# Optimization experiments

Hardware: AMD Instinct MI355X
Metric: run time of the kernel (lower is better)

## Reference

```python
import jax, jax.numpy as jnp
import numpy as np

B, N, F = 8, 1024, 512
H, D = 4, 128  # num_heads, output_dim
LEAKY_ALPHA = 0.2
MASK_VAL = -1e10


def setup_inputs() -> dict:
    key = jax.random.key(0)
    ks = jax.random.split(key, 6)
    X = jax.random.normal(ks[0], (B, N, F), dtype=jnp.float32)
    A = (jax.random.uniform(ks[1], (B, N, N)) < 0.05).astype(jnp.float32)
    A = jnp.maximum(A, jnp.eye(N, dtype=jnp.float32)[None])
    W_att = jax.random.normal(ks[2], (H, F, D), dtype=jnp.float32) * (1.0 / np.sqrt(F))
    a_att = jax.random.normal(ks[3], (H, 2, D), dtype=jnp.float32) * (1.0 / np.sqrt(D))
    kernel = jax.random.normal(ks[4], (H, F, D), dtype=jnp.float32) * (1.0 / np.sqrt(F))
    bias = jax.random.normal(ks[5], (H * D,), dtype=jnp.float32) * 0.02
    return {"X": X, "A": A, "W_att": W_att, "a_att": a_att, "kernel": kernel, "bias": bias}


def reference(X, A, W_att, a_att, kernel, bias):
    # Per-head feature projection used only for attention scores: [H,B,N,D]
    xf = jnp.einsum('bnf,hfd->hbnd', X, W_att)
    att_self = jnp.einsum('hbnd,hd->hbn', xf, a_att[:, 0])       # [H,B,N]
    att_neigh = jnp.einsum('hbnd,hd->hbn', xf, a_att[:, 1])      # [H,B,N]
    # additive scores: scores[h,b,i,j] = self[i] + neigh[j]
    scores = att_self[..., :, None] + att_neigh[..., None, :]    # [H,B,N,N]
    scores = jnp.where(scores >= 0, scores, LEAKY_ALPHA * scores)
    scores = scores + MASK_VAL * (1.0 - A)[None]                 # adjacency mask
    attn = jax.nn.softmax(scores, axis=-1)                       # [H,B,N,N]
    # aggregate raw features X, then per-head kernel projection
    agg = jnp.einsum('hbij,bjf->hbif', attn, X)                  # [H,B,N,F]
    out = jnp.einsum('hbnf,hfd->bnhd', agg, kernel)              # [B,N,H,D]
    out = out.reshape(out.shape[0], out.shape[1], -1)            # concat heads -> [B,N,H*D]
    out = out + bias
    return jax.nn.elu(out)
```

## Files before the change

kernel.cpp:

```cpp
#include <hip/hip_runtime.h>
#include <hip/hip_bf16.h>
#include <math.h>

namespace {
constexpr int B = 8, N = 1024, F = 512, H = 4, D = 128, HD = H * D;
constexpr int ROWS = B * N;
constexpr float LEAKY = 0.2f;

constexpr size_t UV_OFF  = 0;
constexpr size_t ATT_OFF = 4096;
constexpr size_t Y_OFF   = 69632;
constexpr size_t XB_OFF  = 2166784;
constexpr size_t WKB_OFF = 4263936;
}

typedef __attribute__((ext_vector_type(8))) short short8;
typedef __attribute__((ext_vector_type(4))) float f32x4;

__device__ __forceinline__ ushort bf16bits(float x) {
    __hip_bfloat16 h = __float2bfloat16(x);
    return *reinterpret_cast<ushort*>(&h);
}
__device__ __forceinline__ float blo(uint u) {
    return __uint_as_float(u << 16);
}
__device__ __forceinline__ float bhi(uint u) {
    return __uint_as_float(u & 0xffff0000u);
}

extern "C" __global__ __launch_bounds__(256) void k_pre(
    const float* __restrict__ Watt, const float* __restrict__ aatt,
    const float* __restrict__ Wk, float* __restrict__ uv,
    __hip_bfloat16* __restrict__ Wkb) {
    __shared__ ushort T[128][136];
    if (blockIdx.x < 16) {
        int h = blockIdx.x >> 2, f0 = (blockIdx.x & 3) * 128;
#pragma unroll
        for (int p = 0; p < 16; ++p) {
            int fi = p * 8 + (threadIdx.x >> 5);
            int d4 = (threadIdx.x & 31) * 4;
            float4 v = *reinterpret_cast<const float4*>(
                Wk + ((size_t)h * F + f0 + fi) * D + d4);
            T[d4 + 0][fi] = bf16bits(v.x);
            T[d4 + 1][fi] = bf16bits(v.y);
            T[d4 + 2][fi] = bf16bits(v.z);
            T[d4 + 3][fi] = bf16bits(v.w);
        }
        __syncthreads();
        int d = threadIdx.x >> 1, hf = threadIdx.x & 1;
        ushort* dst =
            (ushort*)Wkb + (size_t)(h * 128 + d) * F + f0 + hf * 64;
        const ushort* src = &T[d][hf * 64];
#pragma unroll
        for (int q = 0; q < 8; ++q)
            *reinterpret_cast<uint4*>(dst + q * 8) =
                *reinterpret_cast<const uint4*>(src + q * 8);
    } else {
        int t = (blockIdx.x - 16) * 256 + threadIdx.x;
        int f = t % F;
        int h = (t / F) % H;
        int w = t / (F * H);
        const float* Wrow = Watt + (size_t)(h * F + f) * D;
        const float* arow = aatt + (size_t)(h * 2 + w) * D;
        float s = 0.f;
#pragma unroll 4
        for (int d = 0; d < D; ++d) s = fmaf(Wrow[d], arow[d], s);
        uv[(size_t)w * (H * F) + h * F + f] = s;
    }
}

extern "C" __global__ __launch_bounds__(256) void k_att(
    const float* __restrict__ X, const float* __restrict__ uv,
    float* __restrict__ att, __hip_bfloat16* __restrict__ Xb) {
    int wave = threadIdx.x >> 6, lane = threadIdx.x & 63;
    int row = blockIdx.x * 4 + wave;
    const float4* xr = reinterpret_cast<const float4*>(X + (size_t)row * F);
    float4 v0 = xr[lane * 2], v1 = xr[lane * 2 + 1];

    union { short8 s; __hip_bfloat16 h[8]; } pk;
    pk.h[0] = __float2bfloat16(v0.x); pk.h[1] = __float2bfloat16(v0.y);
    pk.h[2] = __float2bfloat16(v0.z); pk.h[3] = __float2bfloat16(v0.w);
    pk.h[4] = __float2bfloat16(v1.x); pk.h[5] = __float2bfloat16(v1.y);
    pk.h[6] = __float2bfloat16(v1.z); pk.h[7] = __float2bfloat16(v1.w);
    *reinterpret_cast<short8*>(Xb + (size_t)row * F + lane * 8) = pk.s;

    float acc[2][H];
#pragma unroll
    for (int w = 0; w < 2; ++w)
#pragma unroll
        for (int h = 0; h < H; ++h) {
            const float4* up = reinterpret_cast<const float4*>(
                uv + (size_t)w * (H * F) + h * F + lane * 8);
            float4 u0 = up[0], u1 = up[1];
            float a = 0.f;
            a = fmaf(v0.x, u0.x, a); a = fmaf(v0.y, u0.y, a);
            a = fmaf(v0.z, u0.z, a); a = fmaf(v0.w, u0.w, a);
            a = fmaf(v1.x, u1.x, a); a = fmaf(v1.y, u1.y, a);
            a = fmaf(v1.z, u1.z, a); a = fmaf(v1.w, u1.w, a);
            acc[w][h] = a;
        }
#pragma unroll
    for (int w = 0; w < 2; ++w)
#pragma unroll
        for (int h = 0; h < H; ++h) {
            float v = acc[w][h];
#pragma unroll
            for (int off = 32; off > 0; off >>= 1) v += __shfl_xor(v, off);
            if (lane == 0) att[(size_t)w * (H * ROWS) + h * ROWS + row] = v;
        }
}

extern "C" __global__ __launch_bounds__(256) void k_gemm(
    const __hip_bfloat16* __restrict__ Xb,
    const __hip_bfloat16* __restrict__ Wkb,
    __hip_bfloat16* __restrict__ Y) {
    __shared__ __align__(16) char smem[16384];
    int tid = threadIdx.x;
    int lane = tid & 63, wv = tid >> 6;
    int wr = wv >> 1, wc = wv & 1;
    int lt = (blockIdx.x & 7) * 128 + (blockIdx.x >> 3);
    int bm = lt >> 3, bn = lt & 7;
    int row0 = bm * 64, col0 = bn * 64;

    const ushort* Ag = (const ushort*)Xb;
    const ushort* Bg = (const ushort*)Wkb;

    int aoff[2][2], boff[2][2];
#pragma unroll
    for (int ks = 0; ks < 2; ++ks) {
        int cb = ks * 4 + (lane >> 4);
#pragma unroll
        for (int i = 0; i < 2; ++i) {
            int ra = wr * 32 + i * 16 + (lane & 15);
            aoff[i][ks] = ra * 128 + (cb ^ (ra & 7)) * 16;
            int rb = wc * 32 + i * 16 + (lane & 15);
            boff[i][ks] = 8192 + rb * 128 + (cb ^ (rb & 7)) * 16;
        }
    }
    int srow[2], sgb[2];
#pragma unroll
    for (int i = 0; i < 2; ++i) {
        srow[i] = i * 32 + wv * 8 + (lane >> 3);
        sgb[i] = (lane & 7) ^ (srow[i] & 7);
    }

    f32x4 acc[2][2] = {};
    for (int k0 = 0; k0 < F; k0 += 64) {
        __syncthreads();
#pragma unroll
        for (int i = 0; i < 2; ++i) {
            const ushort* ga = Ag + (size_t)(row0 + srow[i]) * F + k0 + sgb[i] * 8;
            __builtin_amdgcn_global_load_lds(
                (const __attribute__((address_space(1))) uint32_t*)ga,
                (__attribute__((address_space(3))) uint32_t*)(smem + wv * 1024 + i * 4096),
                16, 0, 0);
            const ushort* gb = Bg + (size_t)(col0 + srow[i]) * F + k0 + sgb[i] * 8;
            __builtin_amdgcn_global_load_lds(
                (const __attribute__((address_space(1))) uint32_t*)gb,
                (__attribute__((address_space(3))) uint32_t*)(smem + 8192 + wv * 1024 + i * 4096),
                16, 0, 0);
        }
        __syncthreads();
#pragma unroll
        for (int ks = 0; ks < 2; ++ks) {
            short8 af[2], bf[2];
#pragma unroll
            for (int i = 0; i < 2; ++i) {
                af[i] = *reinterpret_cast<short8*>(smem + aoff[i][ks]);
                bf[i] = *reinterpret_cast<short8*>(smem + boff[i][ks]);
            }
#pragma unroll
            for (int mi = 0; mi < 2; ++mi)
#pragma unroll
                for (int ni = 0; ni < 2; ++ni)
                    acc[mi][ni] = __builtin_amdgcn_mfma_f32_16x16x32_bf16(
                        af[mi], bf[ni], acc[mi][ni], 0, 0, 0);
        }
    }
    int cr = (lane >> 4) * 4, cc = lane & 15;
#pragma unroll
    for (int mi = 0; mi < 2; ++mi)
#pragma unroll
        for (int ni = 0; ni < 2; ++ni) {
            int gr = row0 + wr * 32 + mi * 16 + cr;
            int gc = col0 + wc * 32 + ni * 16 + cc;
#pragma unroll
            for (int r = 0; r < 4; ++r)
                Y[(size_t)(gr + r) * HD + gc] =
                    __float2bfloat16(acc[mi][ni][r]);
        }
}

extern "C" __global__ __launch_bounds__(256) void k_attn_agg(
    const float* __restrict__ A, const float* __restrict__ att,
    const ushort* __restrict__ Y, const float* __restrict__ bias,
    float* __restrict__ out) {
    int g = blockIdx.x;
    int bi = ((g & 7) << 10) | (g >> 3);
    int b = bi >> 10;
    int tid = threadIdx.x;
    int lane = tid & 63, wv = tid >> 6;
    __shared__ int idxs[N];
    __shared__ int2 ent[H][256];
    __shared__ int wsum[4];

    const float* Arow = A + (size_t)bi * N;
    float4 av = *reinterpret_cast<const float4*>(Arow + tid * 4);
    int cnt = (av.x != 0.f) + (av.y != 0.f) + (av.z != 0.f) + (av.w != 0.f);
    int isc = cnt;
#pragma unroll
    for (int off = 1; off < 64; off <<= 1) {
        int t = __shfl_up(isc, off);
        if (lane >= off) isc += t;
    }
    if (lane == 63) wsum[wv] = isc;
    __syncthreads();
    int prefix = 0;
#pragma unroll
    for (int wj = 0; wj < 4; ++wj) prefix += (wj < wv) ? wsum[wj] : 0;
    int nnz = wsum[0] + wsum[1] + wsum[2] + wsum[3];
    int wo = prefix + isc - cnt;
    int jb = tid * 4;
    if (av.x != 0.f) idxs[wo++] = jb;
    if (av.y != 0.f) idxs[wo++] = jb + 1;
    if (av.z != 0.f) idxs[wo++] = jb + 2;
    if (av.w != 0.f) idxs[wo++] = jb + 3;
    __syncthreads();

    int h = wv;
    int grp = lane >> 4, sub = lane & 15;
    float sself = att[(size_t)h * ROWS + bi];
    const float* nrow = att + (size_t)(H + h) * ROWS + (size_t)b * N;
    const char* Ybyte = (const char*)(Y + ((size_t)b * N) * HD + h * D + sub * 8);

    float m = -1e30f, l = 0.f;
    float acc[8] = {};
    for (int c0 = 0; c0 < nnz; c0 += 256) {
        int cn = min(256, nnz - c0);
        int kpad = (cn + 15) & ~15;
        float lm = -1e30f;
        for (int k = lane; k < cn; k += 64) {
            int idx = idxs[c0 + k];
            float s = sself + nrow[idx];
            s = s >= 0.f ? s : LEAKY * s;
            ent[h][k] = make_int2(idx << 10, __float_as_int(s));
            lm = fmaxf(lm, s);
        }
        for (int k = cn + lane; k < kpad; k += 64) ent[h][k] = make_int2(0, 0);
#pragma unroll
        for (int off = 32; off > 0; off >>= 1)
            lm = fmaxf(lm, __shfl_xor(lm, off));
        float mn = fmaxf(m, lm);
        float scale = __expf(m - mn);
        float ls = 0.f;
        for (int k = lane; k < cn; k += 64) {
            int2 p = ent[h][k];
            float e = __expf(__int_as_float(p.y) - mn);
            ent[h][k].y = __float_as_int(e);
            ls += e;
        }
#pragma unroll
        for (int off = 32; off > 0; off >>= 1) ls += __shfl_xor(ls, off);
        l = fmaf(l, scale, ls);
#pragma unroll
        for (int q = 0; q < 8; ++q) acc[q] *= scale;
        m = mn;
        for (int k = 0; k < kpad; k += 16) {
            int2 p[4];
#pragma unroll
            for (int q = 0; q < 4; ++q) p[q] = ent[h][k + q * 4 + grp];
            uint4 y[4];
#pragma unroll
            for (int q = 0; q < 4; ++q)
                y[q] = *reinterpret_cast<const uint4*>(Ybyte + (size_t)(uint)p[q].x);
#pragma unroll
            for (int q = 0; q < 4; ++q) {
                float w = __int_as_float(p[q].y);
                acc[0] = fmaf(w, blo(y[q].x), acc[0]);
                acc[1] = fmaf(w, bhi(y[q].x), acc[1]);
                acc[2] = fmaf(w, blo(y[q].y), acc[2]);
                acc[3] = fmaf(w, bhi(y[q].y), acc[3]);
                acc[4] = fmaf(w, blo(y[q].z), acc[4]);
                acc[5] = fmaf(w, bhi(y[q].z), acc[5]);
                acc[6] = fmaf(w, blo(y[q].w), acc[6]);
                acc[7] = fmaf(w, bhi(y[q].w), acc[7]);
            }
        }
    }
#pragma unroll
    for (int q = 0; q < 8; ++q) {
        acc[q] += __shfl_xor(acc[q], 16);
        acc[q] += __shfl_xor(acc[q], 32);
    }
    if (grp == 0) {
        float inv = 1.f / l;
        int cbase = h * D + sub * 8;
        float4 b0 = *reinterpret_cast<const float4*>(bias + cbase);
        float4 b1 = *reinterpret_cast<const float4*>(bias + cbase + 4);
        float o[8];
        o[0] = acc[0] * inv + b0.x; o[1] = acc[1] * inv + b0.y;
        o[2] = acc[2] * inv + b0.z; o[3] = acc[3] * inv + b0.w;
        o[4] = acc[4] * inv + b1.x; o[5] = acc[5] * inv + b1.y;
        o[6] = acc[6] * inv + b1.z; o[7] = acc[7] * inv + b1.w;
#pragma unroll
        for (int q = 0; q < 8; ++q) o[q] = o[q] > 0.f ? o[q] : expm1f(o[q]);
        float* op = out + (size_t)bi * HD + cbase;
        *reinterpret_cast<float4*>(op) = make_float4(o[0], o[1], o[2], o[3]);
        *reinterpret_cast<float4*>(op + 4) = make_float4(o[4], o[5], o[6], o[7]);
    }
}

extern "C" void kernel_launch(void* const* d_in, const int* in_sizes, int n_in,
                              void* d_out, int out_size, void* d_ws,
                              size_t ws_size, hipStream_t stream) {
    const float* X    = (const float*)d_in[0];
    const float* A    = (const float*)d_in[1];
    const float* Watt = (const float*)d_in[2];
    const float* aatt = (const float*)d_in[3];
    const float* Wk   = (const float*)d_in[4];
    const float* bias = (const float*)d_in[5];
    float* out = (float*)d_out;
    float* ws  = (float*)d_ws;

    float* uv  = ws + UV_OFF;
    float* att = ws + ATT_OFF;
    __hip_bfloat16* Yb  = (__hip_bfloat16*)(ws + Y_OFF);
    __hip_bfloat16* Xb  = (__hip_bfloat16*)(ws + XB_OFF);
    __hip_bfloat16* Wkb = (__hip_bfloat16*)(ws + WKB_OFF);

    hipLaunchKernelGGL(k_pre, dim3(32), dim3(256), 0, stream, Watt, aatt, Wk,
                       uv, Wkb);
    hipLaunchKernelGGL(k_att, dim3(ROWS / 4), dim3(256), 0, stream, X, uv, att, Xb);
    hipLaunchKernelGGL(k_gemm, dim3((ROWS / 64) * (HD / 64)), dim3(256), 0,
                       stream, Xb, Wkb, Yb);
    hipLaunchKernelGGL(k_attn_agg, dim3(ROWS), dim3(256), 0, stream, A, att,
                       (const ushort*)Yb, bias, out);
}
```

Before: 68.66 us.

## Stage neighbor feature rows into LDS with double-buffered async global_load_lds

The attention-aggregation kernel now loads each neighbor's full feature row across all heads into shared memory with async global-to-LDS loads, double-buffered over blocks of 8 neighbors. The old code had each wave gather its own head's row slice from global memory. Each wave now processes a subset of neighbors for all heads, and partial sums are reduced across waves through shared memory at the end. The goal is coalesced full-row loads and overlap of memory latency with FMAs, at the cost of two block-wide barriers per 8-neighbor step and an extra cross-wave reduction.

```diff
diff --git a/kernel.cpp b/kernel.cpp
--- a/kernel.cpp
+++ b/kernel.cpp
@@ -201,8 +201,12 @@
     int tid = threadIdx.x;
     int lane = tid & 63, wv = tid >> 6;
     __shared__ int idxs[N];
-    __shared__ int2 ent[H][256];
+    __shared__ int joff[256];
+    __shared__ float w4[H][256];
+    __shared__ float scaleS[H];
+    __shared__ float linvS[H];
     __shared__ int wsum[4];
+    __shared__ __align__(16) ushort rowbuf[2][8][512];
 
     const float* Arow = A + (size_t)bi * N;
     float4 av = *reinterpret_cast<const float4*>(Arow + tid * 4);
@@ -227,26 +231,27 @@
     if (av.w != 0.f) idxs[wo++] = jb + 3;
     __syncthreads();
 
-    int h = wv;
-    int grp = lane >> 4, sub = lane & 15;
-    float sself = att[(size_t)h * ROWS + bi];
-    const float* nrow = att + (size_t)(H + h) * ROWS + (size_t)b * N;
-    const char* Ybyte = (const char*)(Y + ((size_t)b * N) * HD + h * D + sub * 8);
+    int hsel = lane >> 4;
+    float sself = att[(size_t)wv * ROWS + bi];
+    const float* nrow = att + (size_t)(H + wv) * ROWS + (size_t)b * N;
+    const char* Ybb = (const char*)(Y + ((size_t)b * N) * HD);
 
     float m = -1e30f, l = 0.f;
     float acc[8] = {};
     for (int c0 = 0; c0 < nnz; c0 += 256) {
         int cn = min(256, nnz - c0);
-        int kpad = (cn + 15) & ~15;
+        int kpad = (cn + 7) & ~7;
         float lm = -1e30f;
         for (int k = lane; k < cn; k += 64) {
             int idx = idxs[c0 + k];
             float s = sself + nrow[idx];
-            s = s >= 0.f ? s : LEAKY * s;
-            ent[h][k] = make_int2(idx << 10, __float_as_int(s));
+            s = fmaxf(s, LEAKY * s);
+            if (wv == 0) joff[k] = idx << 10;
+            w4[wv][k] = s;
             lm = fmaxf(lm, s);
         }
-        for (int k = cn + lane; k < kpad; k += 64) ent[h][k] = make_int2(0, 0);
+        if (wv == 0)
+            for (int k = cn + lane; k < kpad; k += 64) joff[k] = 0;
 #pragma unroll
         for (int off = 32; off > 0; off >>= 1)
             lm = fmaxf(lm, __shfl_xor(lm, off));
@@ -254,59 +259,81 @@
         float scale = __expf(m - mn);
         float ls = 0.f;
         for (int k = lane; k < cn; k += 64) {
-            int2 p = ent[h][k];
-            float e = __expf(__int_as_float(p.y) - mn);
-            ent[h][k].y = __float_as_int(e);
+            float e = __expf(w4[wv][k] - mn);
+            w4[wv][k] = e;
             ls += e;
         }
+        for (int k = cn + lane; k < kpad; k += 64) w4[wv][k] = 0.f;
 #pragma unroll
         for (int off = 32; off > 0; off >>= 1) ls += __shfl_xor(ls, off);
         l = fmaf(l, scale, ls);
-#pragma unroll
-        for (int q = 0; q < 8; ++q) acc[q] *= scale;
+        if (lane == 0) scaleS[wv] = scale;
         m = mn;
-        for (int k = 0; k < kpad; k += 16) {
-            int2 p[4];
-#pragma unroll
-            for (int q = 0; q < 4; ++q) p[q] = ent[h][k + q * 4 + grp];
-            uint4 y[4];
-#pragma unroll
-            for (int q = 0; q < 4; ++q)
-                y[q] = *reinterpret_cast<const uint4*>(Ybyte + (size_t)(uint)p[q].x);
-#pragma unroll
-            for (int q = 0; q < 4; ++q) {
-                float w = __int_as_float(p[q].y);
-                acc[0] = fmaf(w, blo(y[q].x), acc[0]);
-                acc[1] = fmaf(w, bhi(y[q].x), acc[1]);
-                acc[2] = fmaf(w, blo(y[q].y), acc[2]);
-                acc[3] = fmaf(w, bhi(y[q].y), acc[3]);
-                acc[4] = fmaf(w, blo(y[q].z), acc[4]);
-                acc[5] = fmaf(w, bhi(y[q].z), acc[5]);
-                acc[6] = fmaf(w, blo(y[q].w), acc[6]);
-                acc[7] = fmaf(w, bhi(y[q].w), acc[7]);
+        __syncthreads();
+        float sc = scaleS[hsel];
+#pragma unroll
+        for (int q = 0; q < 8; ++q) acc[q] *= sc;
+
+        int nb = kpad >> 3;
+#pragma unroll
+        for (int rr = 0; rr < 2; ++rr) {
+            int k = wv + rr * 4;
+            const char* src = Ybb + (size_t)(uint)joff[k] + lane * 16;
+            __builtin_amdgcn_global_load_lds(
+                (const __attribute__((address_space(1))) uint32_t*)src,
+                (__attribute__((address_space(3))) uint32_t*)&rowbuf[0][wv + rr * 4][0],
+                16, 0, 0);
+        }
+        for (int c = 0; c < nb; ++c) {
+            if (c + 1 < nb) {
+#pragma unroll
+                for (int rr = 0; rr < 2; ++rr) {
+                    int k = (c + 1) * 8 + wv + rr * 4;
+                    const char* src = Ybb + (size_t)(uint)joff[k] + lane * 16;
+                    __builtin_amdgcn_global_load_lds(
+                        (const __attribute__((address_space(1))) uint32_t*)src,
+                        (__attribute__((address_space(3))) uint32_t*)&rowbuf[(c + 1) & 1][wv + rr * 4][0],
+                        16, 0, 0);
+                }
+                asm volatile("s_waitcnt vmcnt(2)" ::: "memory");
+            } else {
+                asm volatile("s_waitcnt vmcnt(0)" ::: "memory");
             }
-        }
-    }
-#pragma unroll
-    for (int q = 0; q < 8; ++q) {
-        acc[q] += __shfl_xor(acc[q], 16);
-        acc[q] += __shfl_xor(acc[q], 32);
-    }
-    if (grp == 0) {
-        float inv = 1.f / l;
-        int cbase = h * D + sub * 8;
-        float4 b0 = *reinterpret_cast<const float4*>(bias + cbase);
-        float4 b1 = *reinterpret_cast<const float4*>(bias + cbase + 4);
-        float o[8];
-        o[0] = acc[0] * inv + b0.x; o[1] = acc[1] * inv + b0.y;
-        o[2] = acc[2] * inv + b0.z; o[3] = acc[3] * inv + b0.w;
-        o[4] = acc[4] * inv + b1.x; o[5] = acc[5] * inv + b1.y;
-        o[6] = acc[6] * inv + b1.z; o[7] = acc[7] * inv + b1.w;
-#pragma unroll
-        for (int q = 0; q < 8; ++q) o[q] = o[q] > 0.f ? o[q] : expm1f(o[q]);
-        float* op = out + (size_t)bi * HD + cbase;
-        *reinterpret_cast<float4*>(op) = make_float4(o[0], o[1], o[2], o[3]);
-        *reinterpret_cast<float4*>(op + 4) = make_float4(o[4], o[5], o[6], o[7]);
+            __syncthreads();
+#pragma unroll
+            for (int rr = 0; rr < 2; ++rr) {
+                int r = wv + rr * 4;
+                float w = w4[hsel][c * 8 + r];
+                uint4 y = *reinterpret_cast<const uint4*>(
+                    &rowbuf[c & 1][r][lane * 8]);
+                acc[0] = fmaf(w, blo(y.x), acc[0]);
+                acc[1] = fmaf(w, bhi(y.x), acc[1]);
+                acc[2] = fmaf(w, blo(y.y), acc[2]);
+                acc[3] = fmaf(w, bhi(y.y), acc[3]);
+                acc[4] = fmaf(w, blo(y.z), acc[4]);
+                acc[5] = fmaf(w, bhi(y.z), acc[5]);
+                acc[6] = fmaf(w, blo(y.w), acc[6]);
+                acc[7] = fmaf(w, bhi(y.w), acc[7]);
+            }
+            __syncthreads();
+        }
+    }
+    if (lane == 0) linvS[wv] = 1.f / l;
+    __syncthreads();
+    float* scr = (float*)rowbuf;
+#pragma unroll
+    for (int q = 0; q < 8; ++q) scr[((wv << 6) + lane) * 8 + q] = acc[q];
+    __syncthreads();
+#pragma unroll
+    for (int s0 = 0; s0 < 2; ++s0) {
+        int s = tid + s0 * 256;
+        int hh = s >> 7, d = s & 127;
+        int ll = (hh << 4) | (d >> 3), q = d & 7;
+        float v = scr[(0 * 64 + ll) * 8 + q] + scr[(1 * 64 + ll) * 8 + q] +
+                  scr[(2 * 64 + ll) * 8 + q] + scr[(3 * 64 + ll) * 8 + q];
+        v = v * linvS[hh] + bias[s];
+        v = v > 0.f ? v : expm1f(v);
+        out[(size_t)bi * HD + s] = v;
     }
 }
 
```

Result: slower. 76.09 us (+10.8%).

## Replace sparse gather aggregation with dense MFMA attention over transposed Y

Applied to the files above, without the earlier changes.

The per-row sparse gather aggregation is replaced by a dense blocked kernel. Each block handles 32 rows of one batch and builds bf16 exp-weights from an adjacency bitmask, then multiplies them against a transposed Y with MFMA across all 1024 neighbours. A stable upper-bound max (self plus max neighbour score) replaces the online softmax rescaling. The GEMM now writes Y transposed so column reads are contiguous. This trades gather latency for dense compute that is roughly 20x redundant at about 5% density, launches only 256 blocks, and quantises the attention weights to bf16.

```diff
diff --git a/kernel.cpp b/kernel.cpp
--- a/kernel.cpp
+++ b/kernel.cpp
@@ -9,7 +9,7 @@
 
 constexpr size_t UV_OFF  = 0;
 constexpr size_t ATT_OFF = 4096;
-constexpr size_t Y_OFF   = 69632;
+constexpr size_t YT_OFF  = 69632;
 constexpr size_t XB_OFF  = 2166784;
 constexpr size_t WKB_OFF = 4263936;
 }
@@ -20,12 +20,6 @@
 __device__ __forceinline__ ushort bf16bits(float x) {
     __hip_bfloat16 h = __float2bfloat16(x);
     return *reinterpret_cast<ushort*>(&h);
-}
-__device__ __forceinline__ float blo(uint u) {
-    return __uint_as_float(u << 16);
-}
-__device__ __forceinline__ float bhi(uint u) {
-    return __uint_as_float(u & 0xffff0000u);
 }
 
 extern "C" __global__ __launch_bounds__(256) void k_pre(
@@ -77,11 +71,11 @@
     const float4* xr = reinterpret_cast<const float4*>(X + (size_t)row * F);
     float4 v0 = xr[lane * 2], v1 = xr[lane * 2 + 1];
 
-    union { short8 s; __hip_bfloat16 h[8]; } pk;
-    pk.h[0] = __float2bfloat16(v0.x); pk.h[1] = __float2bfloat16(v0.y);
-    pk.h[2] = __float2bfloat16(v0.z); pk.h[3] = __float2bfloat16(v0.w);
-    pk.h[4] = __float2bfloat16(v1.x); pk.h[5] = __float2bfloat16(v1.y);
-    pk.h[6] = __float2bfloat16(v1.z); pk.h[7] = __float2bfloat16(v1.w);
+    union { short8 s; ushort u[8]; } pk;
+    pk.u[0] = bf16bits(v0.x); pk.u[1] = bf16bits(v0.y);
+    pk.u[2] = bf16bits(v0.z); pk.u[3] = bf16bits(v0.w);
+    pk.u[4] = bf16bits(v1.x); pk.u[5] = bf16bits(v1.y);
+    pk.u[6] = bf16bits(v1.z); pk.u[7] = bf16bits(v1.w);
     *reinterpret_cast<short8*>(Xb + (size_t)row * F + lane * 8) = pk.s;
 
     float acc[2][H];
@@ -113,7 +107,7 @@
 extern "C" __global__ __launch_bounds__(256) void k_gemm(
     const __hip_bfloat16* __restrict__ Xb,
     const __hip_bfloat16* __restrict__ Wkb,
-    __hip_bfloat16* __restrict__ Y) {
+    ushort* __restrict__ Yt) {
     __shared__ __align__(16) char smem[16384];
     int tid = threadIdx.x;
     int lane = tid & 63, wv = tid >> 6;
@@ -184,129 +178,145 @@
         for (int ni = 0; ni < 2; ++ni) {
             int gr = row0 + wr * 32 + mi * 16 + cr;
             int gc = col0 + wc * 32 + ni * 16 + cc;
-#pragma unroll
-            for (int r = 0; r < 4; ++r)
-                Y[(size_t)(gr + r) * HD + gc] =
-                    __float2bfloat16(acc[mi][ni][r]);
-        }
-}
-
-extern "C" __global__ __launch_bounds__(256) void k_attn_agg(
+            ushort4 pk4 = make_ushort4(
+                bf16bits(acc[mi][ni][0]), bf16bits(acc[mi][ni][1]),
+                bf16bits(acc[mi][ni][2]), bf16bits(acc[mi][ni][3]));
+            *reinterpret_cast<ushort4*>(Yt + (size_t)gc * ROWS + gr) = pk4;
+        }
+}
+
+extern "C" __global__ __launch_bounds__(256, 1) void k_attn_mfma(
     const float* __restrict__ A, const float* __restrict__ att,
-    const ushort* __restrict__ Y, const float* __restrict__ bias,
+    const ushort* __restrict__ Yt, const float* __restrict__ bias,
     float* __restrict__ out) {
     int g = blockIdx.x;
-    int bi = ((g & 7) << 10) | (g >> 3);
-    int b = bi >> 10;
-    int tid = threadIdx.x;
-    int lane = tid & 63, wv = tid >> 6;
-    __shared__ int idxs[N];
-    __shared__ int2 ent[H][256];
-    __shared__ int wsum[4];
-
-    const float* Arow = A + (size_t)bi * N;
-    float4 av = *reinterpret_cast<const float4*>(Arow + tid * 4);
-    int cnt = (av.x != 0.f) + (av.y != 0.f) + (av.z != 0.f) + (av.w != 0.f);
-    int isc = cnt;
-#pragma unroll
-    for (int off = 1; off < 64; off <<= 1) {
-        int t = __shfl_up(isc, off);
-        if (lane >= off) isc += t;
-    }
-    if (lane == 63) wsum[wv] = isc;
+    int b = g & 7, it = g >> 3;
+    int i0 = it * 32;
+    int bi0 = b * 1024 + i0;
+    int tid = threadIdx.x, lane = tid & 63, w = tid >> 6;
+    int hs = lane >> 4, r15 = lane & 15;
+
+    __shared__ float neighS[H][1024];
+    __shared__ uint bitsS[32][33];
+
+    const float* nr = att + (size_t)(H + w) * ROWS + b * 1024;
+    float nmax = -1e30f;
+#pragma unroll
+    for (int q = 0; q < 4; ++q) {
+        float4 v = reinterpret_cast<const float4*>(nr)[lane + q * 64];
+        *reinterpret_cast<float4*>(&neighS[w][(lane + q * 64) * 4]) = v;
+        nmax = fmaxf(fmaxf(fmaxf(nmax, v.x), fmaxf(v.y, v.z)), v.w);
+    }
+#pragma unroll
+    for (int off = 32; off > 0; off >>= 1)
+        nmax = fmaxf(nmax, __shfl_xor(nmax, off));
+
+    float sv = att[(size_t)w * ROWS + bi0 + (lane & 31)];
+    float self0 = __shfl(sv, r15);
+    float self1 = __shfl(sv, 16 + r15);
+    float m0 = self0 + nmax; m0 = fmaxf(m0, LEAKY * m0);
+    float m1 = self1 + nmax; m1 = fmaxf(m1, LEAKY * m1);
+
+    {
+        int row = tid >> 3, seg = tid & 7;
+        const float4* ar = reinterpret_cast<const float4*>(
+            A + (size_t)(bi0 + row) * 1024 + seg * 128);
+        uint wb[4] = {0, 0, 0, 0};
+#pragma unroll 4
+        for (int q = 0; q < 32; ++q) {
+            float4 v = ar[q];
+            uint mk = (v.x != 0.f) | ((v.y != 0.f) << 1) |
+                      ((v.z != 0.f) << 2) | ((v.w != 0.f) << 3);
+            wb[q >> 3] |= mk << ((q & 7) * 4);
+        }
+#pragma unroll
+        for (int q = 0; q < 4; ++q) bitsS[row][seg * 4 + q] = wb[q];
+    }
     __syncthreads();
-    int prefix = 0;
-#pragma unroll
-    for (int wj = 0; wj < 4; ++wj) prefix += (wj < wv) ? wsum[wj] : 0;
-    int nnz = wsum[0] + wsum[1] + wsum[2] + wsum[3];
-    int wo = prefix + isc - cnt;
-    int jb = tid * 4;
-    if (av.x != 0.f) idxs[wo++] = jb;
-    if (av.y != 0.f) idxs[wo++] = jb + 1;
-    if (av.z != 0.f) idxs[wo++] = jb + 2;
-    if (av.w != 0.f) idxs[wo++] = jb + 3;
-    __syncthreads();
-
-    int h = wv;
-    int grp = lane >> 4, sub = lane & 15;
-    float sself = att[(size_t)h * ROWS + bi];
-    const float* nrow = att + (size_t)(H + h) * ROWS + (size_t)b * N;
-    const char* Ybyte = (const char*)(Y + ((size_t)b * N) * HD + h * D + sub * 8);
-
-    float m = -1e30f, l = 0.f;
-    float acc[8] = {};
-    for (int c0 = 0; c0 < nnz; c0 += 256) {
-        int cn = min(256, nnz - c0);
-        int kpad = (cn + 15) & ~15;
-        float lm = -1e30f;
-        for (int k = lane; k < cn; k += 64) {
-            int idx = idxs[c0 + k];
-            float s = sself + nrow[idx];
-            s = s >= 0.f ? s : LEAKY * s;
-            ent[h][k] = make_int2(idx << 10, __float_as_int(s));
-            lm = fmaxf(lm, s);
-        }
-        for (int k = cn + lane; k < kpad; k += 64) ent[h][k] = make_int2(0, 0);
-#pragma unroll
-        for (int off = 32; off > 0; off >>= 1)
-            lm = fmaxf(lm, __shfl_xor(lm, off));
-        float mn = fmaxf(m, lm);
-        float scale = __expf(m - mn);
-        float ls = 0.f;
-        for (int k = lane; k < cn; k += 64) {
-            int2 p = ent[h][k];
-            float e = __expf(__int_as_float(p.y) - mn);
-            ent[h][k].y = __float_as_int(e);
-            ls += e;
-        }
-#pragma unroll
-        for (int off = 32; off > 0; off >>= 1) ls += __shfl_xor(ls, off);
-        l = fmaf(l, scale, ls);
-#pragma unroll
-        for (int q = 0; q < 8; ++q) acc[q] *= scale;
-        m = mn;
-        for (int k = 0; k < kpad; k += 16) {
-            int2 p[4];
-#pragma unroll
-            for (int q = 0; q < 4; ++q) p[q] = ent[h][k + q * 4 + grp];
-            uint4 y[4];
-#pragma unroll
-            for (int q = 0; q < 4; ++q)
-                y[q] = *reinterpret_cast<const uint4*>(Ybyte + (size_t)(uint)p[q].x);
-#pragma unroll
-            for (int q = 0; q < 4; ++q) {
-                float w = __int_as_float(p[q].y);
-                acc[0] = fmaf(w, blo(y[q].x), acc[0]);
-                acc[1] = fmaf(w, bhi(y[q].x), acc[1]);
-                acc[2] = fmaf(w, blo(y[q].y), acc[2]);
-                acc[3] = fmaf(w, bhi(y[q].y), acc[3]);
-                acc[4] = fmaf(w, blo(y[q].z), acc[4]);
-                acc[5] = fmaf(w, bhi(y[q].z), acc[5]);
-                acc[6] = fmaf(w, blo(y[q].w), acc[6]);
-                acc[7] = fmaf(w, bhi(y[q].w), acc[7]);
-            }
-        }
-    }
-#pragma unroll
-    for (int q = 0; q < 8; ++q) {
-        acc[q] += __shfl_xor(acc[q], 16);
-        acc[q] += __shfl_xor(acc[q], 32);
-    }
-    if (grp == 0) {
-        float inv = 1.f / l;
-        int cbase = h * D + sub * 8;
-        float4 b0 = *reinterpret_cast<const float4*>(bias + cbase);
-        float4 b1 = *reinterpret_cast<const float4*>(bias + cbase + 4);
-        float o[8];
-        o[0] = acc[0] * inv + b0.x; o[1] = acc[1] * inv + b0.y;
-        o[2] = acc[2] * inv + b0.z; o[3] = acc[3] * inv + b0.w;
-        o[4] = acc[4] * inv + b1.x; o[5] = acc[5] * inv + b1.y;
-        o[6] = acc[6] * inv + b1.z; o[7] = acc[7] * inv + b1.w;
-#pragma unroll
-        for (int q = 0; q < 8; ++q) o[q] = o[q] > 0.f ? o[q] : expm1f(o[q]);
-        float* op = out + (size_t)bi * HD + cbase;
-        *reinterpret_cast<float4*>(op) = make_float4(o[0], o[1], o[2], o[3]);
-        *reinterpret_cast<float4*>(op + 4) = make_float4(o[4], o[5], o[6], o[7]);
+
+    const ushort* colp[8];
+#pragma unroll
+    for (int ni = 0; ni < 8; ++ni)
+        colp[ni] = Yt + (size_t)(w * 128 + ni * 16 + r15) * ROWS + b * 1024 +
+                   hs * 8;
+
+    f32x4 acc[2][8] = {};
+    float lsum0 = 0.f, lsum1 = 0.f;
+
+    for (int c = 0; c < 8; ++c) {
+        short8 bf[8];
+#pragma unroll
+        for (int ni = 0; ni < 8; ++ni)
+            bf[ni] = *reinterpret_cast<const short8*>(colp[ni] + c * 128);
+
+        short8 pa0[4], pa1[4];
+#pragma unroll
+        for (int kt = 0; kt < 4; ++kt) {
+            int j0 = c * 128 + kt * 32 + hs * 8;
+            float4 n0 = *reinterpret_cast<const float4*>(&neighS[w][j0]);
+            float4 n1 = *reinterpret_cast<const float4*>(&neighS[w][j0 + 4]);
+            float nj[8] = {n0.x, n0.y, n0.z, n0.w, n1.x, n1.y, n1.z, n1.w};
+            uint by0 = (bitsS[r15][c * 4 + kt] >> (hs * 8)) & 0xffu;
+            uint by1 = (bitsS[16 + r15][c * 4 + kt] >> (hs * 8)) & 0xffu;
+            union { short8 s; ushort u[8]; } u0, u1;
+#pragma unroll
+            for (int q = 0; q < 8; ++q) {
+                float s0 = self0 + nj[q]; s0 = fmaxf(s0, LEAKY * s0);
+                float e0 = ((by0 >> q) & 1) ? __expf(s0 - m0) : 0.f;
+                lsum0 += e0; u0.u[q] = bf16bits(e0);
+                float s1 = self1 + nj[q]; s1 = fmaxf(s1, LEAKY * s1);
+                float e1 = ((by1 >> q) & 1) ? __expf(s1 - m1) : 0.f;
+                lsum1 += e1; u1.u[q] = bf16bits(e1);
+            }
+            pa0[kt] = u0.s; pa1[kt] = u1.s;
+        }
+
+#pragma unroll
+        for (int kt = 0; kt < 4; ++kt) {
+            short8 bn[8];
+            if (kt < 3) {
+#pragma unroll
+                for (int ni = 0; ni < 8; ++ni)
+                    bn[ni] = *reinterpret_cast<const short8*>(
+                        colp[ni] + c * 128 + (kt + 1) * 32);
+            }
+#pragma unroll
+            for (int ni = 0; ni < 8; ++ni) {
+                acc[0][ni] = __builtin_amdgcn_mfma_f32_16x16x32_bf16(
+                    pa0[kt], bf[ni], acc[0][ni], 0, 0, 0);
+                acc[1][ni] = __builtin_amdgcn_mfma_f32_16x16x32_bf16(
+                    pa1[kt], bf[ni], acc[1][ni], 0, 0, 0);
+            }
+            if (kt < 3) {
+#pragma unroll
+                for (int ni = 0; ni < 8; ++ni) bf[ni] = bn[ni];
+            }
+        }
+    }
+
+    lsum0 += __shfl_xor(lsum0, 16); lsum0 += __shfl_xor(lsum0, 32);
+    lsum1 += __shfl_xor(lsum1, 16); lsum1 += __shfl_xor(lsum1, 32);
+    float linv0 = 1.f / lsum0, linv1 = 1.f / lsum1;
+    float li[2][4];
+#pragma unroll
+    for (int r = 0; r < 4; ++r) {
+        li[0][r] = __shfl(linv0, hs * 4 + r);
+        li[1][r] = __shfl(linv1, hs * 4 + r);
+    }
+
+#pragma unroll
+    for (int ni = 0; ni < 8; ++ni) {
+        int col = w * 128 + ni * 16 + r15;
+        float bv = bias[col];
+#pragma unroll
+        for (int rt = 0; rt < 2; ++rt)
+#pragma unroll
+            for (int r = 0; r < 4; ++r) {
+                int rowc = rt * 16 + hs * 4 + r;
+                float v = acc[rt][ni][r] * li[rt][r] + bv;
+                v = v > 0.f ? v : expm1f(v);
+                out[(size_t)(bi0 + rowc) * HD + col] = v;
+            }
     }
 }
 
@@ -324,7 +334,7 @@
 
     float* uv  = ws + UV_OFF;
     float* att = ws + ATT_OFF;
-    __hip_bfloat16* Yb  = (__hip_bfloat16*)(ws + Y_OFF);
+    ushort* Yt = (ushort*)(ws + YT_OFF);
     __hip_bfloat16* Xb  = (__hip_bfloat16*)(ws + XB_OFF);
     __hip_bfloat16* Wkb = (__hip_bfloat16*)(ws + WKB_OFF);
 
@@ -332,7 +342,7 @@
                        uv, Wkb);
     hipLaunchKernelGGL(k_att, dim3(ROWS / 4), dim3(256), 0, stream, X, uv, att, Xb);
     hipLaunchKernelGGL(k_gemm, dim3((ROWS / 64) * (HD / 64)), dim3(256), 0,
-                       stream, Xb, Wkb, Yb);
-    hipLaunchKernelGGL(k_attn_agg, dim3(ROWS), dim3(256), 0, stream, A, att,
-                       (const ushort*)Yb, bias, out);
-}
+                       stream, Xb, Wkb, Yt);
+    hipLaunchKernelGGL(k_attn_mfma, dim3(256), dim3(256), 0, stream, A, att,
+                       Yt, bias, out);
+}
```

After: 95.29 us. +38.8%, slower.
